# Kernel tuning notes

Hardware: AMD Instinct MI355X
Metric: run time of the kernel (lower is better)

Reference implementation:

```python
import jax, jax.numpy as jnp
import numpy as np

NUM_HEADS = 32
NUM_KV_HEADS = 8
HEAD_DIM = 128
SCALING = 0.08838834764831845  # 1/sqrt(128)
B, T = 2, 2048


def setup_inputs() -> dict:
    key = jax.random.key(0)
    kq, kk, kv = jax.random.split(key, 3)
    q = jax.random.normal(kq, (B, T, NUM_HEADS, HEAD_DIM), dtype=jnp.float32)
    k = jax.random.normal(kk, (B, T, NUM_KV_HEADS, HEAD_DIM), dtype=jnp.float32)
    v = jax.random.normal(kv, (B, T, NUM_KV_HEADS, HEAD_DIM), dtype=jnp.float32)
    return {"q": q, "k": k, "v": v}


def _attn(q, k, v):
    # GQA expand: [B,T,nKv,D] -> [B,T,nH,D]
    n_rep = NUM_HEADS // NUM_KV_HEADS
    Bq, Tq = q.shape[0], q.shape[1]
    k = jnp.broadcast_to(k[:, :, :, None, :], (Bq, Tq, NUM_KV_HEADS, n_rep, HEAD_DIM)).reshape(Bq, Tq, NUM_HEADS, HEAD_DIM)
    v = jnp.broadcast_to(v[:, :, :, None, :], (Bq, Tq, NUM_KV_HEADS, n_rep, HEAD_DIM)).reshape(Bq, Tq, NUM_HEADS, HEAD_DIM)
    # scores: [B,H,T,T]
    scores = jnp.einsum('bqhd,bkhd->bhqk', q, k) * SCALING
    causal = jnp.triu(jnp.ones((Tq, Tq), dtype=bool), k=1)  # True above diagonal
    scores = jnp.where(causal, jnp.finfo(scores.dtype).min, scores)
    probs = jax.nn.softmax(scores, axis=-1)
    out = jnp.einsum('bhqk,bkhd->bqhd', probs, v)
    return out.reshape(Bq, Tq, NUM_HEADS * HEAD_DIM)


def reference(q, k, v):
    return _attn(q, k, v)
```

## Files before the change

kernel.cpp:

```cpp
#include <hip/hip_runtime.h>
#include <stdint.h>


typedef __attribute__((ext_vector_type(8))) __bf16 bf16x8;
typedef __attribute__((ext_vector_type(16))) float f32x16;

#define QSCALE (0.08838834764831845f * 1.4426950408889634f)

__host__ __device__ inline unsigned pi32(unsigned x) {
    unsigned q2 = (x >> 2) & 3u;
    return (q2 == 1u || q2 == 2u) ? (x ^ 12u) : x;
}

__global__ __launch_bounds__(256) void cvt_k(const float* __restrict__ k,
                                             unsigned short* __restrict__ kb) {
    unsigned tid = blockIdx.x * 256u + threadIdx.x;
    unsigned s = tid & 15u;
    unsigned h = (tid >> 4) & 7u;
    unsigned t = (tid >> 7) & 2047u;
    unsigned b = tid >> 18;
    const float4* src = (const float4*)(k + (size_t)tid * 8u);
    float4 f0 = src[0], f1 = src[1];
    bf16x8 r;
    r[0] = (__bf16)f0.x; r[1] = (__bf16)f0.y; r[2] = (__bf16)f0.z; r[3] = (__bf16)f0.w;
    r[4] = (__bf16)f1.x; r[5] = (__bf16)f1.y; r[6] = (__bf16)f1.z; r[7] = (__bf16)f1.w;
    unsigned tp = (t & ~31u) | pi32(t & 31u);
    size_t o = ((size_t)((b * 8u + h) * 2048u + tp) * 16u + (s ^ (tp & 7u))) * 8u;
    *(bf16x8*)(kb + o) = r;
}

__global__ __launch_bounds__(256) void cvt_v(const float* __restrict__ v,
                                             unsigned short* __restrict__ vtb) {
    unsigned tid = blockIdx.x * 256u + threadIdx.x;
    unsigned d = tid & 127u;
    unsigned oct = (tid >> 7) & 3u;
    unsigned tile = (tid >> 9) & 63u;
    unsigned kvh = (tid >> 15) & 7u;
    unsigned b = tid >> 18;
    const float* src = v + ((size_t)(b * 2048u + tile * 32u + oct * 8u) * 8u + kvh) * 128u + d;
    bf16x8 r;
#pragma unroll
    for (int e = 0; e < 8; ++e) r[e] = (__bf16)src[(size_t)e * 1024u];
    unsigned p = d >> 1;
    unsigned slot = (d & 1u) * 4u + oct;
    size_t off = (size_t)(b * 8u + kvh) * 262144u + (size_t)tile * 4096u
               + (p * 8u + (slot ^ (p & 7u))) * 8u;
    *(bf16x8*)(vtb + off) = r;
}

__device__ inline void load16_lds(const void* g, void* l) {
    __builtin_amdgcn_global_load_lds(
        (__attribute__((address_space(1))) void*)(g),
        (__attribute__((address_space(3))) void*)(l), 16, 0, 0);
}

union BW2 { unsigned u; __bf16 h[2]; };
union BW8 { unsigned u[4]; bf16x8 v; };

__global__ __launch_bounds__(256, 3) void attn_fwd(const float* __restrict__ qg,
                                                   const unsigned short* __restrict__ kb,
                                                   const unsigned short* __restrict__ vtb,
                                                   float* __restrict__ outg) {
    __shared__ __align__(16) unsigned short K0[32 * 128], K1[32 * 128], K2[32 * 128];
    __shared__ __align__(16) unsigned short V0[64 * 64],  V1[64 * 64],  V2[64 * 64];

    int bid = blockIdx.x;
    int kvh = bid & 7;
    int pos = bid >> 3;
    int qt = 15 - (pos >> 3);
    int sub = pos & 7;
    int b = sub & 1;
    int h = kvh * 4 + (sub >> 1);

    int tid = threadIdx.x;
    int lane = tid & 63;
    int lq = lane & 31;
    int hi = lane >> 5;
    int q0w = qt * 128 + (tid >> 6) * 32;
    int nt = 4 * (qt + 1);

    const unsigned short* kT = kb + (size_t)(b * 8 + kvh) * 262144u;
    const unsigned short* vT = vtb + (size_t)(b * 8 + kvh) * 262144u;

    auto stage = [&](int t, unsigned short* kd, unsigned short* vd) {
        const char* ks = (const char*)(kT + (size_t)t * 4096u);
        const char* vs = (const char*)(vT + (size_t)t * 4096u);
#pragma unroll
        for (int i = 0; i < 2; ++i) {
            load16_lds(ks + (i * 256 + tid) * 16, kd + (i * 256 + tid) * 8);
            load16_lds(vs + (i * 256 + tid) * 16, vd + (i * 256 + tid) * 8);
        }
    };

    stage(0, K0, V0);
    stage(1, K1, V1);

    bf16x8 qf[8];
    {
        const float* qp = qg + ((size_t)(b * 2048 + q0w + lq) * 32u + h) * 128u;
#pragma unroll
        for (int c = 0; c < 8; ++c) {
            int d0 = c * 16 + hi * 8;
            float4 f0 = *(const float4*)(qp + d0);
            float4 f1 = *(const float4*)(qp + d0 + 4);
            qf[c][0] = (__bf16)(f0.x * QSCALE); qf[c][1] = (__bf16)(f0.y * QSCALE);
            qf[c][2] = (__bf16)(f0.z * QSCALE); qf[c][3] = (__bf16)(f0.w * QSCALE);
            qf[c][4] = (__bf16)(f1.x * QSCALE); qf[c][5] = (__bf16)(f1.y * QSCALE);
            qf[c][6] = (__bf16)(f1.z * QSCALE); qf[c][7] = (__bf16)(f1.w * QSCALE);
        }
    }

    f32x16 acc[4];
#pragma unroll
    for (int dt = 0; dt < 4; ++dt)
#pragma unroll
        for (int r = 0; r < 16; ++r) acc[dt][r] = 0.f;
    float lrun = 0.f;

    unsigned short *kc = K0, *kn = K1, *kx = K2;
    unsigned short *vc = V0, *vn = V1, *vx = V2;

    for (int t = 0; t < nt; ++t) {
        if (t + 2 < nt) { asm volatile("s_waitcnt vmcnt(4)" ::: "memory"); }
        else            { asm volatile("s_waitcnt vmcnt(0)" ::: "memory"); }
        __builtin_amdgcn_s_barrier();
        if (t + 2 < nt) stage(t + 2, kx, vx);
        int kv0 = t * 32;
        if (kv0 <= q0w + 31) {
            f32x16 st0;
#pragma unroll
            for (int r = 0; r < 16; ++r) st0[r] = 0.f;
            __builtin_amdgcn_s_setprio(1);
#pragma unroll
            for (int c = 0; c < 8; ++c) {
                bf16x8 kf = *(const bf16x8*)&kc[lq * 128 + (((2 * c + hi) ^ (lq & 7)) << 3)];
                st0 = __builtin_amdgcn_mfma_f32_32x32x16_bf16(kf, qf[c], st0, 0, 0, 0);
            }
            __builtin_amdgcn_s_setprio(0);
            if (kv0 == q0w) {
#pragma unroll
                for (int r = 0; r < 16; ++r) {
                    int kvl = (r & 3) + 8 * (r >> 2) + 4 * hi;
                    int q2 = (kvl >> 2) & 3;
                    int kva = (q2 == 1 || q2 == 2) ? (kvl ^ 12) : kvl;
                    if (kva > lq) st0[r] = -1e30f;
                }
            }
#pragma unroll
            for (int r = 0; r < 16; ++r) st0[r] = exp2f(st0[r]);
            BW8 pb0, pb1;
#pragma unroll
            for (int i = 0; i < 4; ++i) {
                BW2 a; a.h[0] = (__bf16)st0[2 * i];     a.h[1] = (__bf16)st0[2 * i + 1];
                BW2 c; c.h[0] = (__bf16)st0[8 + 2 * i]; c.h[1] = (__bf16)st0[9 + 2 * i];
                pb0.u[i] = a.u; pb1.u[i] = c.u;
            }
            __builtin_amdgcn_s_setprio(1);
#pragma unroll
            for (int dt = 0; dt < 4; ++dt) {
                int drow = dt * 32 + lq;
                int pp = drow >> 1;
                int s0 = (drow & 1) * 4 + hi;
                int s1 = s0 + 2;
                bf16x8 vf0 = *(const bf16x8*)&vc[pp * 64 + ((s0 ^ (pp & 7)) << 3)];
                acc[dt] = __builtin_amdgcn_mfma_f32_32x32x16_bf16(vf0, pb0.v, acc[dt], 0, 0, 0);
                bf16x8 vf1 = *(const bf16x8*)&vc[pp * 64 + ((s1 ^ (pp & 7)) << 3)];
                acc[dt] = __builtin_amdgcn_mfma_f32_32x32x16_bf16(vf1, pb1.v, acc[dt], 0, 0, 0);
            }
            __builtin_amdgcn_s_setprio(0);
            float s8[8];
#pragma unroll
            for (int i = 0; i < 8; ++i) s8[i] = st0[2 * i] + st0[2 * i + 1];
#pragma unroll
            for (int i = 0; i < 4; ++i) s8[i] = s8[i] + s8[i + 4];
            lrun += (s8[0] + s8[1]) + (s8[2] + s8[3]);
        }
        unsigned short* tk = kc; kc = kn; kn = kx; kx = tk;
        unsigned short* tv = vc; vc = vn; vn = vx; vx = tv;
    }

    lrun += __shfl_xor(lrun, 32);
    float il = 1.0f / lrun;
    float* ob = outg + ((size_t)(b * 2048 + q0w + lq) * 32u + h) * 128u;
#pragma unroll
    for (int dt = 0; dt < 4; ++dt)
#pragma unroll
        for (int rq = 0; rq < 4; ++rq) {
            int d = dt * 32 + rq * 8 + hi * 4;
            float4 o4 = { acc[dt][rq * 4 + 0] * il, acc[dt][rq * 4 + 1] * il,
                          acc[dt][rq * 4 + 2] * il, acc[dt][rq * 4 + 3] * il };
            *(float4*)(ob + d) = o4;
        }
}

extern "C" void kernel_launch(void* const* d_in, const int* in_sizes, int n_in,
                              void* d_out, int out_size, void* d_ws, size_t ws_size,
                              hipStream_t stream) {
    const float* q = (const float*)d_in[0];
    const float* k = (const float*)d_in[1];
    const float* v = (const float*)d_in[2];
    float* out = (float*)d_out;
    unsigned short* kbuf = (unsigned short*)d_ws;
    unsigned short* vbuf = kbuf + (size_t)2 * 8 * 2048 * 128;
    cvt_k<<<2048, 256, 0, stream>>>(k, kbuf);
    cvt_v<<<2048, 256, 0, stream>>>(v, vbuf);
    attn_fwd<<<1024, 256, 0, stream>>>(q, kbuf, vbuf, out);
}
```

Before: 110.4 us.

## Spill scaled Q fragments to global scratch to cut registers and raise occupancy

Adds a variant kernel that writes the scaled bf16 Q fragments to a workspace buffer and reloads them from global memory on every QK step instead of holding them in registers. It also drops from triple to double LDS buffering, which lowers LDS use and allows launch_bounds occupancy of 4. Loads of Q are repeated every iteration through cache, and the shallower pipeline waits vmcnt(0) each step, which may expose memory latency. The original register version is kept as a fallback when the workspace is too small.

```diff
diff --git a/kernel.cpp b/kernel.cpp
--- a/kernel.cpp
+++ b/kernel.cpp
@@ -57,12 +57,13 @@
 union BW2 { unsigned u; __bf16 h[2]; };
 union BW8 { unsigned u[4]; bf16x8 v; };
 
-__global__ __launch_bounds__(256, 3) void attn_fwd(const float* __restrict__ qg,
-                                                   const unsigned short* __restrict__ kb,
-                                                   const unsigned short* __restrict__ vtb,
-                                                   float* __restrict__ outg) {
-    __shared__ __align__(16) unsigned short K0[32 * 128], K1[32 * 128], K2[32 * 128];
-    __shared__ __align__(16) unsigned short V0[64 * 64],  V1[64 * 64],  V2[64 * 64];
+__global__ __launch_bounds__(256, 4) void attn_qs(const float* __restrict__ qg,
+                                                  const unsigned short* __restrict__ kb,
+                                                  const unsigned short* __restrict__ vtb,
+                                                  unsigned short* qsc,
+                                                  float* __restrict__ outg) {
+    __shared__ __align__(16) unsigned short K0[32 * 128], K1[32 * 128];
+    __shared__ __align__(16) unsigned short V0[64 * 64],  V1[64 * 64];
 
     int bid = blockIdx.x;
     int kvh = bid & 7;
@@ -74,28 +75,16 @@
 
     int tid = threadIdx.x;
     int lane = tid & 63;
+    int w = tid >> 6;
     int lq = lane & 31;
     int hi = lane >> 5;
-    int q0w = qt * 128 + (tid >> 6) * 32;
+    int q0w = qt * 128 + w * 32;
     int nt = 4 * (qt + 1);
 
     const unsigned short* kT = kb + (size_t)(b * 8 + kvh) * 262144u;
     const unsigned short* vT = vtb + (size_t)(b * 8 + kvh) * 262144u;
-
-    auto stage = [&](int t, unsigned short* kd, unsigned short* vd) {
-        const char* ks = (const char*)(kT + (size_t)t * 4096u);
-        const char* vs = (const char*)(vT + (size_t)t * 4096u);
-#pragma unroll
-        for (int i = 0; i < 2; ++i) {
-            load16_lds(ks + (i * 256 + tid) * 16, kd + (i * 256 + tid) * 8);
-            load16_lds(vs + (i * 256 + tid) * 16, vd + (i * 256 + tid) * 8);
-        }
-    };
-
-    stage(0, K0, V0);
-    stage(1, K1, V1);
-
-    bf16x8 qf[8];
+    unsigned short* qwbw = qsc + (size_t)(((b * 32 + h) * 16 + qt) * 4 + w) * 4096u;
+
     {
         const float* qp = qg + ((size_t)(b * 2048 + q0w + lq) * 32u + h) * 128u;
 #pragma unroll
@@ -103,12 +92,28 @@
             int d0 = c * 16 + hi * 8;
             float4 f0 = *(const float4*)(qp + d0);
             float4 f1 = *(const float4*)(qp + d0 + 4);
-            qf[c][0] = (__bf16)(f0.x * QSCALE); qf[c][1] = (__bf16)(f0.y * QSCALE);
-            qf[c][2] = (__bf16)(f0.z * QSCALE); qf[c][3] = (__bf16)(f0.w * QSCALE);
-            qf[c][4] = (__bf16)(f1.x * QSCALE); qf[c][5] = (__bf16)(f1.y * QSCALE);
-            qf[c][6] = (__bf16)(f1.z * QSCALE); qf[c][7] = (__bf16)(f1.w * QSCALE);
-        }
-    }
+            bf16x8 r;
+            r[0] = (__bf16)(f0.x * QSCALE); r[1] = (__bf16)(f0.y * QSCALE);
+            r[2] = (__bf16)(f0.z * QSCALE); r[3] = (__bf16)(f0.w * QSCALE);
+            r[4] = (__bf16)(f1.x * QSCALE); r[5] = (__bf16)(f1.y * QSCALE);
+            r[6] = (__bf16)(f1.z * QSCALE); r[7] = (__bf16)(f1.w * QSCALE);
+            *(bf16x8*)(qwbw + ((c * 2 + hi) * 32 + lq) * 8) = r;
+        }
+    }
+    asm volatile("s_waitcnt vmcnt(0)" ::: "memory");
+    const unsigned short* qwb = qwbw;
+
+    auto stage = [&](int t, unsigned short* kd, unsigned short* vd) {
+        const char* ks = (const char*)(kT + (size_t)t * 4096u);
+        const char* vs = (const char*)(vT + (size_t)t * 4096u);
+#pragma unroll
+        for (int i = 0; i < 2; ++i) {
+            load16_lds(ks + (i * 256 + tid) * 16, kd + (i * 256 + tid) * 8);
+            load16_lds(vs + (i * 256 + tid) * 16, vd + (i * 256 + tid) * 8);
+        }
+    };
+
+    stage(0, K0, V0);
 
     f32x16 acc[4];
 #pragma unroll
@@ -117,14 +122,13 @@
         for (int r = 0; r < 16; ++r) acc[dt][r] = 0.f;
     float lrun = 0.f;
 
-    unsigned short *kc = K0, *kn = K1, *kx = K2;
-    unsigned short *vc = V0, *vn = V1, *vx = V2;
+    unsigned short *kc = K0, *kn = K1;
+    unsigned short *vc = V0, *vn = V1;
 
     for (int t = 0; t < nt; ++t) {
-        if (t + 2 < nt) { asm volatile("s_waitcnt vmcnt(4)" ::: "memory"); }
-        else            { asm volatile("s_waitcnt vmcnt(0)" ::: "memory"); }
+        asm volatile("s_waitcnt vmcnt(0)" ::: "memory");
         __builtin_amdgcn_s_barrier();
-        if (t + 2 < nt) stage(t + 2, kx, vx);
+        if (t + 1 < nt) stage(t + 1, kn, vn);
         int kv0 = t * 32;
         if (kv0 <= q0w + 31) {
             f32x16 st0;
@@ -133,8 +137,9 @@
             __builtin_amdgcn_s_setprio(1);
 #pragma unroll
             for (int c = 0; c < 8; ++c) {
+                bf16x8 qc = *(const bf16x8*)(qwb + ((c * 2 + hi) * 32 + lq) * 8);
                 bf16x8 kf = *(const bf16x8*)&kc[lq * 128 + (((2 * c + hi) ^ (lq & 7)) << 3)];
-                st0 = __builtin_amdgcn_mfma_f32_32x32x16_bf16(kf, qf[c], st0, 0, 0, 0);
+                st0 = __builtin_amdgcn_mfma_f32_32x32x16_bf16(kf, qc, st0, 0, 0, 0);
             }
             __builtin_amdgcn_s_setprio(0);
             if (kv0 == q0w) {
@@ -175,6 +180,142 @@
             for (int i = 0; i < 4; ++i) s8[i] = s8[i] + s8[i + 4];
             lrun += (s8[0] + s8[1]) + (s8[2] + s8[3]);
         }
+        unsigned short* tk = kc; kc = kn; kn = tk;
+        unsigned short* tv = vc; vc = vn; vn = tv;
+    }
+
+    lrun += __shfl_xor(lrun, 32);
+    float il = 1.0f / lrun;
+    float* ob = outg + ((size_t)(b * 2048 + q0w + lq) * 32u + h) * 128u;
+#pragma unroll
+    for (int dt = 0; dt < 4; ++dt)
+#pragma unroll
+        for (int rq = 0; rq < 4; ++rq) {
+            int d = dt * 32 + rq * 8 + hi * 4;
+            float4 o4 = { acc[dt][rq * 4 + 0] * il, acc[dt][rq * 4 + 1] * il,
+                          acc[dt][rq * 4 + 2] * il, acc[dt][rq * 4 + 3] * il };
+            *(float4*)(ob + d) = o4;
+        }
+}
+
+__global__ __launch_bounds__(256, 3) void attn_reg(const float* __restrict__ qg,
+                                                   const unsigned short* __restrict__ kb,
+                                                   const unsigned short* __restrict__ vtb,
+                                                   float* __restrict__ outg) {
+    __shared__ __align__(16) unsigned short K0[32 * 128], K1[32 * 128], K2[32 * 128];
+    __shared__ __align__(16) unsigned short V0[64 * 64],  V1[64 * 64],  V2[64 * 64];
+
+    int bid = blockIdx.x;
+    int kvh = bid & 7;
+    int pos = bid >> 3;
+    int qt = 15 - (pos >> 3);
+    int sub = pos & 7;
+    int b = sub & 1;
+    int h = kvh * 4 + (sub >> 1);
+
+    int tid = threadIdx.x;
+    int lane = tid & 63;
+    int lq = lane & 31;
+    int hi = lane >> 5;
+    int q0w = qt * 128 + (tid >> 6) * 32;
+    int nt = 4 * (qt + 1);
+
+    const unsigned short* kT = kb + (size_t)(b * 8 + kvh) * 262144u;
+    const unsigned short* vT = vtb + (size_t)(b * 8 + kvh) * 262144u;
+
+    auto stage = [&](int t, unsigned short* kd, unsigned short* vd) {
+        const char* ks = (const char*)(kT + (size_t)t * 4096u);
+        const char* vs = (const char*)(vT + (size_t)t * 4096u);
+#pragma unroll
+        for (int i = 0; i < 2; ++i) {
+            load16_lds(ks + (i * 256 + tid) * 16, kd + (i * 256 + tid) * 8);
+            load16_lds(vs + (i * 256 + tid) * 16, vd + (i * 256 + tid) * 8);
+        }
+    };
+
+    stage(0, K0, V0);
+    stage(1, K1, V1);
+
+    bf16x8 qf[8];
+    {
+        const float* qp = qg + ((size_t)(b * 2048 + q0w + lq) * 32u + h) * 128u;
+#pragma unroll
+        for (int c = 0; c < 8; ++c) {
+            int d0 = c * 16 + hi * 8;
+            float4 f0 = *(const float4*)(qp + d0);
+            float4 f1 = *(const float4*)(qp + d0 + 4);
+            qf[c][0] = (__bf16)(f0.x * QSCALE); qf[c][1] = (__bf16)(f0.y * QSCALE);
+            qf[c][2] = (__bf16)(f0.z * QSCALE); qf[c][3] = (__bf16)(f0.w * QSCALE);
+            qf[c][4] = (__bf16)(f1.x * QSCALE); qf[c][5] = (__bf16)(f1.y * QSCALE);
+            qf[c][6] = (__bf16)(f1.z * QSCALE); qf[c][7] = (__bf16)(f1.w * QSCALE);
+        }
+    }
+
+    f32x16 acc[4];
+#pragma unroll
+    for (int dt = 0; dt < 4; ++dt)
+#pragma unroll
+        for (int r = 0; r < 16; ++r) acc[dt][r] = 0.f;
+    float lrun = 0.f;
+
+    unsigned short *kc = K0, *kn = K1, *kx = K2;
+    unsigned short *vc = V0, *vn = V1, *vx = V2;
+
+    for (int t = 0; t < nt; ++t) {
+        if (t + 2 < nt) { asm volatile("s_waitcnt vmcnt(4)" ::: "memory"); }
+        else            { asm volatile("s_waitcnt vmcnt(0)" ::: "memory"); }
+        __builtin_amdgcn_s_barrier();
+        if (t + 2 < nt) stage(t + 2, kx, vx);
+        int kv0 = t * 32;
+        if (kv0 <= q0w + 31) {
+            f32x16 st0;
+#pragma unroll
+            for (int r = 0; r < 16; ++r) st0[r] = 0.f;
+            __builtin_amdgcn_s_setprio(1);
+#pragma unroll
+            for (int c = 0; c < 8; ++c) {
+                bf16x8 kf = *(const bf16x8*)&kc[lq * 128 + (((2 * c + hi) ^ (lq & 7)) << 3)];
+                st0 = __builtin_amdgcn_mfma_f32_32x32x16_bf16(kf, qf[c], st0, 0, 0, 0);
+            }
+            __builtin_amdgcn_s_setprio(0);
+            if (kv0 == q0w) {
+#pragma unroll
+                for (int r = 0; r < 16; ++r) {
+                    int kvl = (r & 3) + 8 * (r >> 2) + 4 * hi;
+                    int q2 = (kvl >> 2) & 3;
+                    int kva = (q2 == 1 || q2 == 2) ? (kvl ^ 12) : kvl;
+                    if (kva > lq) st0[r] = -1e30f;
+                }
+            }
+#pragma unroll
+            for (int r = 0; r < 16; ++r) st0[r] = exp2f(st0[r]);
+            BW8 pb0, pb1;
+#pragma unroll
+            for (int i = 0; i < 4; ++i) {
+                BW2 a; a.h[0] = (__bf16)st0[2 * i];     a.h[1] = (__bf16)st0[2 * i + 1];
+                BW2 c; c.h[0] = (__bf16)st0[8 + 2 * i]; c.h[1] = (__bf16)st0[9 + 2 * i];
+                pb0.u[i] = a.u; pb1.u[i] = c.u;
+            }
+            __builtin_amdgcn_s_setprio(1);
+#pragma unroll
+            for (int dt = 0; dt < 4; ++dt) {
+                int drow = dt * 32 + lq;
+                int pp = drow >> 1;
+                int s0 = (drow & 1) * 4 + hi;
+                int s1 = s0 + 2;
+                bf16x8 vf0 = *(const bf16x8*)&vc[pp * 64 + ((s0 ^ (pp & 7)) << 3)];
+                acc[dt] = __builtin_amdgcn_mfma_f32_32x32x16_bf16(vf0, pb0.v, acc[dt], 0, 0, 0);
+                bf16x8 vf1 = *(const bf16x8*)&vc[pp * 64 + ((s1 ^ (pp & 7)) << 3)];
+                acc[dt] = __builtin_amdgcn_mfma_f32_32x32x16_bf16(vf1, pb1.v, acc[dt], 0, 0, 0);
+            }
+            __builtin_amdgcn_s_setprio(0);
+            float s8[8];
+#pragma unroll
+            for (int i = 0; i < 8; ++i) s8[i] = st0[2 * i] + st0[2 * i + 1];
+#pragma unroll
+            for (int i = 0; i < 4; ++i) s8[i] = s8[i] + s8[i + 4];
+            lrun += (s8[0] + s8[1]) + (s8[2] + s8[3]);
+        }
         unsigned short* tk = kc; kc = kn; kn = kx; kx = tk;
         unsigned short* tv = vc; vc = vn; vn = vx; vx = tv;
     }
@@ -201,8 +342,14 @@
     const float* v = (const float*)d_in[2];
     float* out = (float*)d_out;
     unsigned short* kbuf = (unsigned short*)d_ws;
-    unsigned short* vbuf = kbuf + (size_t)2 * 8 * 2048 * 128;
+    unsigned short* vbuf = kbuf + (size_t)4194304;
+    unsigned short* qbuf = vbuf + (size_t)4194304;
+    const size_t need = ((size_t)4194304 * 2 + (size_t)16777216) * 2;
     cvt_k<<<2048, 256, 0, stream>>>(k, kbuf);
     cvt_v<<<2048, 256, 0, stream>>>(v, vbuf);
-    attn_fwd<<<1024, 256, 0, stream>>>(q, kbuf, vbuf, out);
-}
+    if (ws_size >= need) {
+        attn_qs<<<1024, 256, 0, stream>>>(q, kbuf, vbuf, qbuf, out);
+    } else {
+        attn_reg<<<1024, 256, 0, stream>>>(q, kbuf, vbuf, out);
+    }
+}
```

After: 203.8 us. 1.85x slower.

## Split attention into producer QK/softmax waves and consumer PV waves

Applied to the files above, without the earlier changes.

Launches 512-thread blocks where four waves compute QK^T scores and exp2 probabilities, write them to a double-buffered LDS tile, and four other waves run the PV MFMAs one tile behind. A fourth V buffer holds the V tile the consumers are still reading, and the row sums travel through LDS for the final normalization. The aim is to overlap score/exp work with the PV matrix multiplies across separate waves. In exchange it adds LDS traffic for P, costs extra LDS per block, and lowers occupancy to 2 blocks per CU.

```diff
diff --git a/kernel.cpp b/kernel.cpp
--- a/kernel.cpp
+++ b/kernel.cpp
@@ -57,12 +57,14 @@
 union BW2 { unsigned u; __bf16 h[2]; };
 union BW8 { unsigned u[4]; bf16x8 v; };
 
-__global__ __launch_bounds__(256, 3) void attn_fwd(const float* __restrict__ qg,
+__global__ __launch_bounds__(512, 2) void attn_fwd(const float* __restrict__ qg,
                                                    const unsigned short* __restrict__ kb,
                                                    const unsigned short* __restrict__ vtb,
                                                    float* __restrict__ outg) {
-    __shared__ __align__(16) unsigned short K0[32 * 128], K1[32 * 128], K2[32 * 128];
-    __shared__ __align__(16) unsigned short V0[64 * 64],  V1[64 * 64],  V2[64 * 64];
+    __shared__ __align__(16) unsigned short K0[32*128], K1[32*128], K2[32*128];
+    __shared__ __align__(16) unsigned short V0[64*64], V1[64*64], V2[64*64], V3[64*64];
+    __shared__ __align__(16) unsigned short Pl[2][4][1024];
+    __shared__ float lsum[4][64];
 
     int bid = blockIdx.x;
     int kvh = bid & 7;
@@ -74,9 +76,12 @@
 
     int tid = threadIdx.x;
     int lane = tid & 63;
+    int w = tid >> 6;
+    int pw = w & 3;
+    bool isP = (w < 4);
     int lq = lane & 31;
     int hi = lane >> 5;
-    int q0w = qt * 128 + (tid >> 6) * 32;
+    int q0w = qt * 128 + pw * 32;
     int nt = 4 * (qt + 1);
 
     const unsigned short* kT = kb + (size_t)(b * 8 + kvh) * 262144u;
@@ -85,18 +90,12 @@
     auto stage = [&](int t, unsigned short* kd, unsigned short* vd) {
         const char* ks = (const char*)(kT + (size_t)t * 4096u);
         const char* vs = (const char*)(vT + (size_t)t * 4096u);
-#pragma unroll
-        for (int i = 0; i < 2; ++i) {
-            load16_lds(ks + (i * 256 + tid) * 16, kd + (i * 256 + tid) * 8);
-            load16_lds(vs + (i * 256 + tid) * 16, vd + (i * 256 + tid) * 8);
-        }
+        load16_lds(ks + tid * 16, kd + tid * 8);
+        load16_lds(vs + tid * 16, vd + tid * 8);
     };
 
-    stage(0, K0, V0);
-    stage(1, K1, V1);
-
     bf16x8 qf[8];
-    {
+    if (isP) {
         const float* qp = qg + ((size_t)(b * 2048 + q0w + lq) * 32u + h) * 128u;
 #pragma unroll
         for (int c = 0; c < 8; ++c) {
@@ -110,87 +109,111 @@
         }
     }
 
+    stage(0, K0, V0);
+    stage(1, K1, V1);
+
     f32x16 acc[4];
-#pragma unroll
-    for (int dt = 0; dt < 4; ++dt)
-#pragma unroll
-        for (int r = 0; r < 16; ++r) acc[dt][r] = 0.f;
+    if (!isP) {
+#pragma unroll
+        for (int dt = 0; dt < 4; ++dt)
+#pragma unroll
+            for (int r = 0; r < 16; ++r) acc[dt][r] = 0.f;
+    }
     float lrun = 0.f;
 
-    unsigned short *kc = K0, *kn = K1, *kx = K2;
-    unsigned short *vc = V0, *vn = V1, *vx = V2;
-
-    for (int t = 0; t < nt; ++t) {
-        if (t + 2 < nt) { asm volatile("s_waitcnt vmcnt(4)" ::: "memory"); }
+    unsigned short *k0 = K0, *k1 = K1, *k2 = K2;
+    unsigned short *vm1 = V3, *v0 = V0, *v1 = V1, *v2 = V2;
+
+    for (int t = 0; t <= nt; ++t) {
+        if (t + 1 < nt) { asm volatile("s_waitcnt vmcnt(2)" ::: "memory"); }
         else            { asm volatile("s_waitcnt vmcnt(0)" ::: "memory"); }
+        asm volatile("s_waitcnt lgkmcnt(0)" ::: "memory");
         __builtin_amdgcn_s_barrier();
-        if (t + 2 < nt) stage(t + 2, kx, vx);
-        int kv0 = t * 32;
-        if (kv0 <= q0w + 31) {
-            f32x16 st0;
-#pragma unroll
-            for (int r = 0; r < 16; ++r) st0[r] = 0.f;
-            __builtin_amdgcn_s_setprio(1);
-#pragma unroll
-            for (int c = 0; c < 8; ++c) {
-                bf16x8 kf = *(const bf16x8*)&kc[lq * 128 + (((2 * c + hi) ^ (lq & 7)) << 3)];
-                st0 = __builtin_amdgcn_mfma_f32_32x32x16_bf16(kf, qf[c], st0, 0, 0, 0);
+        if (t + 2 < nt) stage(t + 2, k2, v2);
+        if (isP) {
+            int kv0 = t * 32;
+            if (kv0 <= q0w + 31) {
+                f32x16 st0;
+#pragma unroll
+                for (int r = 0; r < 16; ++r) st0[r] = 0.f;
+                __builtin_amdgcn_s_setprio(1);
+#pragma unroll
+                for (int c = 0; c < 8; ++c) {
+                    bf16x8 kf = *(const bf16x8*)&k0[lq * 128 + (((2 * c + hi) ^ (lq & 7)) << 3)];
+                    st0 = __builtin_amdgcn_mfma_f32_32x32x16_bf16(kf, qf[c], st0, 0, 0, 0);
+                }
+                __builtin_amdgcn_s_setprio(0);
+                if (kv0 == q0w) {
+#pragma unroll
+                    for (int r = 0; r < 16; ++r) {
+                        int kvl = (r & 3) + 8 * (r >> 2) + 4 * hi;
+                        int q2 = (kvl >> 2) & 3;
+                        int kva = (q2 == 1 || q2 == 2) ? (kvl ^ 12) : kvl;
+                        if (kva > lq) st0[r] = -1e30f;
+                    }
+                }
+#pragma unroll
+                for (int r = 0; r < 16; ++r) st0[r] = exp2f(st0[r]);
+                BW8 pb0, pb1;
+#pragma unroll
+                for (int i = 0; i < 4; ++i) {
+                    BW2 a; a.h[0] = (__bf16)st0[2 * i];     a.h[1] = (__bf16)st0[2 * i + 1];
+                    BW2 c; c.h[0] = (__bf16)st0[8 + 2 * i]; c.h[1] = (__bf16)st0[9 + 2 * i];
+                    pb0.u[i] = a.u; pb1.u[i] = c.u;
+                }
+                *(bf16x8*)&Pl[t & 1][pw][lane * 8] = pb0.v;
+                *(bf16x8*)&Pl[t & 1][pw][512 + lane * 8] = pb1.v;
+                float s8[8];
+#pragma unroll
+                for (int i = 0; i < 8; ++i) s8[i] = st0[2 * i] + st0[2 * i + 1];
+#pragma unroll
+                for (int i = 0; i < 4; ++i) s8[i] = s8[i] + s8[i + 4];
+                lrun += (s8[0] + s8[1]) + (s8[2] + s8[3]);
             }
-            __builtin_amdgcn_s_setprio(0);
-            if (kv0 == q0w) {
-#pragma unroll
-                for (int r = 0; r < 16; ++r) {
-                    int kvl = (r & 3) + 8 * (r >> 2) + 4 * hi;
-                    int q2 = (kvl >> 2) & 3;
-                    int kva = (q2 == 1 || q2 == 2) ? (kvl ^ 12) : kvl;
-                    if (kva > lq) st0[r] = -1e30f;
-                }
+        } else {
+            int tp = t - 1;
+            if (tp >= 0 && tp * 32 <= q0w + 31) {
+                BW8 pb0, pb1;
+                pb0.v = *(const bf16x8*)&Pl[tp & 1][pw][lane * 8];
+                pb1.v = *(const bf16x8*)&Pl[tp & 1][pw][512 + lane * 8];
+                __builtin_amdgcn_s_setprio(1);
+#pragma unroll
+                for (int dt = 0; dt < 4; ++dt) {
+                    int drow = dt * 32 + lq;
+                    int pp = drow >> 1;
+                    int s0 = (drow & 1) * 4 + hi;
+                    int s1 = s0 + 2;
+                    bf16x8 vf0 = *(const bf16x8*)&vm1[pp * 64 + ((s0 ^ (pp & 7)) << 3)];
+                    acc[dt] = __builtin_amdgcn_mfma_f32_32x32x16_bf16(vf0, pb0.v, acc[dt], 0, 0, 0);
+                    bf16x8 vf1 = *(const bf16x8*)&vm1[pp * 64 + ((s1 ^ (pp & 7)) << 3)];
+                    acc[dt] = __builtin_amdgcn_mfma_f32_32x32x16_bf16(vf1, pb1.v, acc[dt], 0, 0, 0);
+                }
+                __builtin_amdgcn_s_setprio(0);
             }
-#pragma unroll
-            for (int r = 0; r < 16; ++r) st0[r] = exp2f(st0[r]);
-            BW8 pb0, pb1;
-#pragma unroll
-            for (int i = 0; i < 4; ++i) {
-                BW2 a; a.h[0] = (__bf16)st0[2 * i];     a.h[1] = (__bf16)st0[2 * i + 1];
-                BW2 c; c.h[0] = (__bf16)st0[8 + 2 * i]; c.h[1] = (__bf16)st0[9 + 2 * i];
-                pb0.u[i] = a.u; pb1.u[i] = c.u;
+        }
+        unsigned short* tk = k0; k0 = k1; k1 = k2; k2 = tk;
+        unsigned short* tv = vm1; vm1 = v0; v0 = v1; v1 = v2; v2 = tv;
+    }
+
+    if (isP) {
+        lrun += __shfl_xor(lrun, 32);
+        lsum[pw][lane] = lrun;
+    }
+    asm volatile("s_waitcnt lgkmcnt(0)" ::: "memory");
+    __builtin_amdgcn_s_barrier();
+    if (!isP) {
+        float il = 1.0f / lsum[pw][lane];
+        float* ob = outg + ((size_t)(b * 2048 + q0w + lq) * 32u + h) * 128u;
+#pragma unroll
+        for (int dt = 0; dt < 4; ++dt)
+#pragma unroll
+            for (int rq = 0; rq < 4; ++rq) {
+                int d = dt * 32 + rq * 8 + hi * 4;
+                float4 o4 = { acc[dt][rq * 4 + 0] * il, acc[dt][rq * 4 + 1] * il,
+                              acc[dt][rq * 4 + 2] * il, acc[dt][rq * 4 + 3] * il };
+                *(float4*)(ob + d) = o4;
             }
-            __builtin_amdgcn_s_setprio(1);
-#pragma unroll
-            for (int dt = 0; dt < 4; ++dt) {
-                int drow = dt * 32 + lq;
-                int pp = drow >> 1;
-                int s0 = (drow & 1) * 4 + hi;
-                int s1 = s0 + 2;
-                bf16x8 vf0 = *(const bf16x8*)&vc[pp * 64 + ((s0 ^ (pp & 7)) << 3)];
-                acc[dt] = __builtin_amdgcn_mfma_f32_32x32x16_bf16(vf0, pb0.v, acc[dt], 0, 0, 0);
-                bf16x8 vf1 = *(const bf16x8*)&vc[pp * 64 + ((s1 ^ (pp & 7)) << 3)];
-                acc[dt] = __builtin_amdgcn_mfma_f32_32x32x16_bf16(vf1, pb1.v, acc[dt], 0, 0, 0);
-            }
-            __builtin_amdgcn_s_setprio(0);
-            float s8[8];
-#pragma unroll
-            for (int i = 0; i < 8; ++i) s8[i] = st0[2 * i] + st0[2 * i + 1];
-#pragma unroll
-            for (int i = 0; i < 4; ++i) s8[i] = s8[i] + s8[i + 4];
-            lrun += (s8[0] + s8[1]) + (s8[2] + s8[3]);
-        }
-        unsigned short* tk = kc; kc = kn; kn = kx; kx = tk;
-        unsigned short* tv = vc; vc = vn; vn = vx; vx = tv;
-    }
-
-    lrun += __shfl_xor(lrun, 32);
-    float il = 1.0f / lrun;
-    float* ob = outg + ((size_t)(b * 2048 + q0w + lq) * 32u + h) * 128u;
-#pragma unroll
-    for (int dt = 0; dt < 4; ++dt)
-#pragma unroll
-        for (int rq = 0; rq < 4; ++rq) {
-            int d = dt * 32 + rq * 8 + hi * 4;
-            float4 o4 = { acc[dt][rq * 4 + 0] * il, acc[dt][rq * 4 + 1] * il,
-                          acc[dt][rq * 4 + 2] * il, acc[dt][rq * 4 + 3] * il };
-            *(float4*)(ob + d) = o4;
-        }
+    }
 }
 
 extern "C" void kernel_launch(void* const* d_in, const int* in_sizes, int n_in,
@@ -204,5 +227,5 @@
     unsigned short* vbuf = kbuf + (size_t)2 * 8 * 2048 * 128;
     cvt_k<<<2048, 256, 0, stream>>>(k, kbuf);
     cvt_v<<<2048, 256, 0, stream>>>(v, vbuf);
-    attn_fwd<<<1024, 256, 0, stream>>>(q, kbuf, vbuf, out);
-}
+    attn_fwd<<<1024, 512, 0, stream>>>(q, kbuf, vbuf, out);
+}
```

After: 161.5 us. 1.46x slower.
